# Kernel optimization log

Hardware: AMD Instinct MI355X
Metric: run time of the kernel (lower is better)

## Reference

```python
import jax, jax.numpy as jnp
import numpy as np

N_HEADS = 1
D_MODEL = 128
TOP_K = 64
BATCH = 4
SEQ = 4096


def _rope_tables(T, d_head):
    # div_term = 10000**(arange(0,d,2)/d), repeat_interleave(2); even slice recovers the base freqs
    pos = jnp.arange(T, dtype=jnp.float32)[:, None]            # (T,1)
    div = 10000.0 ** (jnp.arange(0, d_head, 2, dtype=jnp.float32) / d_head)  # (d/2,)
    ang = pos / div[None, :]                                    # (T, d/2)
    return jnp.cos(ang), jnp.sin(ang)


def _apply_rope(x, cos, sin):
    # x: (..., T, d); cos/sin: (T, d/2) broadcast over leading dims
    xe = x[..., 0::2]
    xo = x[..., 1::2]
    re = xe * cos - xo * sin
    ro = xe * sin + xo * cos
    return jnp.stack([re, ro], axis=-1).reshape(x.shape)


def setup_inputs() -> dict:
    key = jax.random.key(0)
    kq, kk, kv = jax.random.split(key, 3)
    q = jax.random.normal(kq, (BATCH, SEQ, D_MODEL), dtype=jnp.float32)
    k = jax.random.normal(kk, (BATCH, SEQ, D_MODEL), dtype=jnp.float32)
    v = jax.random.normal(kv, (BATCH, SEQ, D_MODEL), dtype=jnp.float32)
    return {"q": q, "k": k, "v": v}


def reference(q, k, v):
    b, T, d_model = q.shape
    H = N_HEADS
    D = d_model // H  # d_head; module only valid for H=1 (k is never head-split)
    qh = q.reshape(b, T, H, D).transpose(0, 2, 1, 3)   # (b,H,T,D)
    vh = v.reshape(b, T, H, D).transpose(0, 2, 1, 3)   # (b,H,T,D)
    kh = k[:, None, :, :]                              # (b,1,T,d_model) == (b,H,T,D) for H=1

    cos, sin = _rope_tables(T, D)
    qh = _apply_rope(qh, cos, sin)
    kh = _apply_rope(kh, cos, sin)

    scale = 1.0 / jnp.sqrt(jnp.asarray(D, dtype=qh.dtype))
    logits = jnp.einsum('bhtd,bhsd->bhts', qh, kh) * scale   # (b,H,T,T)

    idx = jnp.arange(T)
    causal = idx[None, :] <= idx[:, None]                    # (T,T): key j <= query i
    logits = jnp.where(causal[None, None], logits, -jnp.inf)

    topk_vals, topk_idx = jax.lax.top_k(logits, TOP_K)       # (b,H,T,K)
    attn = jax.nn.softmax(topk_vals, axis=-1)                # -inf rows -> 0 weight

    bi = jnp.arange(b)[:, None, None, None]
    hi = jnp.arange(H)[None, :, None, None]
    topk_v = vh[bi, hi, topk_idx]                            # (b,H,T,K,D)
    out = jnp.einsum('bhtk,bhtkd->bhtd', attn, topk_v)       # (b,H,T,D)
    return out.transpose(0, 2, 1, 3).reshape(b, T, d_model)
```

## Files before the change

### kernel.cpp

```cpp
#include <hip/hip_runtime.h>
#include <math.h>

#define BATCH 4
#define SEQ   4096
#define DM    128
#define TOPK  64
#define SCALE 0.08838834764831845f
#define CAP   384

typedef short bf16x8 __attribute__((ext_vector_type(8)));
typedef float f32x4  __attribute__((ext_vector_type(4)));

__device__ __forceinline__ unsigned short f2bf(float x) {
    unsigned u = __float_as_uint(x);
    u += 0x7FFFu + ((u >> 16) & 1u);
    return (unsigned short)(u >> 16);
}
__device__ __forceinline__ float bf2f(unsigned short h) {
    return __uint_as_float(((unsigned)h) << 16);
}
__device__ __forceinline__ void split3(float x, unsigned short& h,
                                       unsigned short& md, unsigned short& l) {
    h = f2bf(x);
    float r1 = x - bf2f(h);
    md = f2bf(r1);
    float r2 = r1 - bf2f(md);
    l = f2bf(r2);
}

__device__ __forceinline__ unsigned fmap(float f) {
    unsigned u = __float_as_uint(f);
    return (u & 0x80000000u) ? ~u : (u | 0x80000000u);
}
__device__ __forceinline__ float finv(unsigned u) {
    return (u & 0x80000000u) ? __uint_as_float(u & 0x7FFFFFFFu) : __uint_as_float(~u);
}
__device__ __forceinline__ float wave_fmax(float v) {
    #pragma unroll
    for (int m = 32; m; m >>= 1) v = fmaxf(v, __shfl_xor(v, m));
    return v;
}
__device__ __forceinline__ float wave_fsum(float v) {
    #pragma unroll
    for (int m = 32; m; m >>= 1) v += __shfl_xor(v, m);
    return v;
}
__device__ __forceinline__ int wave_isum(int v) {
    #pragma unroll
    for (int m = 32; m; m >>= 1) v += __shfl_xor(v, m);
    return v;
}
__device__ __forceinline__ unsigned wave_umax(unsigned v) {
    #pragma unroll
    for (int m = 32; m; m >>= 1) { unsigned o = __shfl_xor(v, m); v = (o > v) ? o : v; }
    return v;
}

__global__ void rope_decomp(const float* __restrict__ q, const float* __restrict__ k,
                            unsigned short* __restrict__ qh, unsigned short* __restrict__ qm,
                            unsigned short* __restrict__ ql, unsigned short* __restrict__ kh,
                            unsigned short* __restrict__ km, unsigned short* __restrict__ kl) {
    int idx = blockIdx.x * blockDim.x + threadIdx.x;
    const int total = BATCH * SEQ * (DM / 2);
    if (idx >= total) return;
    int i   = idx & 63;
    int pos = (idx >> 6) & (SEQ - 1);
    int b   = idx >> 18;
    float dv  = powf(10000.0f, (float)(2 * i) / (float)DM);
    float ang = (float)pos / dv;
    float sn, cs;
    sincosf(ang, &sn, &cs);
    size_t base = ((size_t)b * SEQ + pos) * DM + 2 * i;
    float qe = q[base], qo = q[base + 1];
    float ke = k[base], ko = k[base + 1];
    float q0 = (qe * cs - qo * sn) * SCALE, q1 = (qe * sn + qo * cs) * SCALE;
    float k0 = ke * cs - ko * sn,          k1 = ke * sn + ko * cs;
    unsigned short h, m2, l;
    split3(q0, h, m2, l); qh[base] = h;     qm[base] = m2;     ql[base] = l;
    split3(q1, h, m2, l); qh[base + 1] = h; qm[base + 1] = m2; ql[base + 1] = l;
    split3(k0, h, m2, l); kh[base] = h;     km[base] = m2;     kl[base] = l;
    split3(k1, h, m2, l); kh[base + 1] = h; km[base + 1] = m2; kl[base + 1] = l;
}

__launch_bounds__(256, 2)
__global__ void logits_mfma(const unsigned short* __restrict__ qh, const unsigned short* __restrict__ qm,
                            const unsigned short* __restrict__ ql, const unsigned short* __restrict__ kh,
                            const unsigned short* __restrict__ km, const unsigned short* __restrict__ kl,
                            float* __restrict__ lg, int r0, int m, int stride) {
    const int st = blockIdx.x, qt = blockIdx.y, b = blockIdx.z;
    const int Q0 = r0 + qt * 128, S0 = st * 128;
    if (S0 > Q0 + 127) return;
    const int tid = threadIdx.x, lane = tid & 63, w = tid >> 6;
    const int wm = (w >> 1) * 64, wn = (w & 1) * 64;
    if (S0 + wn > Q0 + wm + 63) return;

    const int rA = Q0 + wm + (lane & 15);
    const int rB = S0 + wn + (lane & 15);
    const int dc = (lane >> 4) * 8;

    f32x4 acc[4][4] = {};
    #pragma unroll
    for (int kk = 0; kk < 4; ++kk) {
        const int doff = kk * 32 + dc;
        bf16x8 Ah[4], Am[4], Al[4], Bh[4], Bm[4], Bl[4];
        #pragma unroll
        for (int i = 0; i < 4; ++i) {
            size_t qoff = ((size_t)b * SEQ + rA + i * 16) * DM + doff;
            Ah[i] = *(const bf16x8*)(qh + qoff);
            Am[i] = *(const bf16x8*)(qm + qoff);
            Al[i] = *(const bf16x8*)(ql + qoff);
            size_t koff = ((size_t)b * SEQ + rB + i * 16) * DM + doff;
            Bh[i] = *(const bf16x8*)(kh + koff);
            Bm[i] = *(const bf16x8*)(km + koff);
            Bl[i] = *(const bf16x8*)(kl + koff);
        }
        #pragma unroll
        for (int i = 0; i < 4; ++i)
            #pragma unroll
            for (int j = 0; j < 4; ++j) {
                f32x4 c = acc[i][j];
                c = __builtin_amdgcn_mfma_f32_16x16x32_bf16(Ah[i], Bh[j], c, 0, 0, 0);
                c = __builtin_amdgcn_mfma_f32_16x16x32_bf16(Ah[i], Bm[j], c, 0, 0, 0);
                c = __builtin_amdgcn_mfma_f32_16x16x32_bf16(Am[i], Bh[j], c, 0, 0, 0);
                c = __builtin_amdgcn_mfma_f32_16x16x32_bf16(Ah[i], Bl[j], c, 0, 0, 0);
                c = __builtin_amdgcn_mfma_f32_16x16x32_bf16(Al[i], Bh[j], c, 0, 0, 0);
                c = __builtin_amdgcn_mfma_f32_16x16x32_bf16(Am[i], Bm[j], c, 0, 0, 0);
                acc[i][j] = c;
            }
    }

    const int colb = lane & 15, rowb = (lane >> 4) * 4;
    #pragma unroll
    for (int i = 0; i < 4; ++i) {
        #pragma unroll
        for (int r = 0; r < 4; ++r) {
            int qrow = Q0 + wm + i * 16 + rowb + r;
            size_t base = ((size_t)(b * m + (qrow - r0))) * stride;
            #pragma unroll
            for (int j = 0; j < 4; ++j) {
                int col = S0 + wn + j * 16 + colb;
                if (col <= qrow) lg[base + col] = acc[i][j][r];
            }
        }
    }
}

__launch_bounds__(256)
__global__ void select_out2(const float* __restrict__ lg, const float* __restrict__ v,
                            float* __restrict__ out, int r0, int m, int stride) {
    __shared__ unsigned long long bufK[4][CAP];
    __shared__ float sW[4][TOPK];
    __shared__ int   sI[4][TOPK];
    __shared__ int   cnt[4];

    const int w = threadIdx.x >> 6, lane = threadIdx.x & 63;
    const int x = blockIdx.x * 4 + w, b = blockIdx.y;
    if (x >= m) return;
    const int t = r0 + x, n = t + 1;
    const float* row = lg + ((size_t)(b * m + x)) * stride;
    const float4* row4 = (const float4*)row;
    const int nv4 = n >> 2, rem = n & 3;

    if (n <= TOPK) {
        float val = (lane < n) ? row[lane] : -3.0e38f;
        float M = wave_fmax(val);
        float wgt = (lane < n) ? expf(val - M) : 0.f;
        float S = wave_fsum(wgt);
        sW[w][lane] = wgt;
        float inv = 1.f / S;
        float a0 = 0.f, a1 = 0.f;
        for (int j = 0; j < n; ++j) {
            float wj = sW[w][j];
            size_t base = ((size_t)b * SEQ + j) * DM;
            a0 += wj * v[base + lane];
            a1 += wj * v[base + 64 + lane];
        }
        size_t ob = ((size_t)b * SEQ + t) * DM;
        out[ob + lane] = a0 * inv;
        out[ob + 64 + lane] = a1 * inv;
        return;
    }

    float T;
    if (n <= 300) {
        T = -3.0e38f;
    } else {
        float p  = 128.f / (float)n;
        float tt = sqrtf(-2.f * logf(p));
        T = tt - (2.30753f + 0.27061f * tt) / (1.f + 0.99229f * tt + 0.04481f * tt * tt);
    }

    unsigned um = 0u;
    float Tlo = -3.3e38f, Thi = 3.3e38f;
    int C = 0;
    for (int it = 0; it < 24; ++it) {
        int c = 0;
        unsigned lm = 0u;
        for (int i = lane; i < nv4; i += 64) {
            float4 r4 = row4[i];
            c += (r4.x >= T) + (r4.y >= T) + (r4.z >= T) + (r4.w >= T);
            if (it == 0) {
                unsigned u0 = fmap(r4.x), u1 = fmap(r4.y), u2 = fmap(r4.z), u3 = fmap(r4.w);
                unsigned a = u0 > u1 ? u0 : u1, bb = u2 > u3 ? u2 : u3;
                a = a > bb ? a : bb;
                lm = a > lm ? a : lm;
            }
        }
        if (lane < rem) {
            float val = row[nv4 * 4 + lane];
            c += (val >= T);
            if (it == 0) { unsigned u = fmap(val); lm = u > lm ? u : lm; }
        }
        C = wave_isum(c);
        if (it == 0) um = wave_umax(lm);
        if (C >= TOPK && C <= CAP) break;
        if (C < TOPK) Thi = T; else Tlo = T;
        if (Tlo > -3.2e38f && Thi < 3.2e38f) T = 0.5f * (Tlo + Thi);
        else if (C < TOPK)                   T = T - 0.45f;
        else                                 T = T + 0.35f;
    }
    const float M = finv(um);

    if (lane == 0) cnt[w] = 0;
    for (int i = lane; i < nv4; i += 64) {
        float4 r4 = row4[i];
        int s = i << 2;
        if (r4.x >= T) { int p = atomicAdd(&cnt[w], 1); if (p < CAP) bufK[w][p] = ((unsigned long long)fmap(r4.x) << 32) | (unsigned)(SEQ - s); }
        if (r4.y >= T) { int p = atomicAdd(&cnt[w], 1); if (p < CAP) bufK[w][p] = ((unsigned long long)fmap(r4.y) << 32) | (unsigned)(SEQ - (s + 1)); }
        if (r4.z >= T) { int p = atomicAdd(&cnt[w], 1); if (p < CAP) bufK[w][p] = ((unsigned long long)fmap(r4.z) << 32) | (unsigned)(SEQ - (s + 2)); }
        if (r4.w >= T) { int p = atomicAdd(&cnt[w], 1); if (p < CAP) bufK[w][p] = ((unsigned long long)fmap(r4.w) << 32) | (unsigned)(SEQ - (s + 3)); }
    }
    if (lane < rem) {
        float val = row[nv4 * 4 + lane];
        if (val >= T) { int p = atomicAdd(&cnt[w], 1); if (p < CAP) bufK[w][p] = ((unsigned long long)fmap(val) << 32) | (unsigned)(SEQ - (nv4 * 4 + lane)); }
    }
    int Cw = cnt[w];
    if (Cw > CAP) Cw = CAP;

    for (int c0 = lane; c0 < Cw; c0 += 64) {
        unsigned long long kc = bufK[w][c0];
        int r = 0;
        for (int j = 0; j < Cw; ++j) r += (bufK[w][j] > kc);
        if (r < TOPK) {
            sW[w][r] = expf(finv((unsigned)(kc >> 32)) - M);
            sI[w][r] = SEQ - (int)(kc & 0xFFFFFFFFu);
        }
    }

    float S = wave_fsum(sW[w][lane]);
    float inv = 1.f / S;

    float a0 = 0.f, a1 = 0.f;
    #pragma unroll 4
    for (int j = 0; j < TOPK; ++j) {
        float wj = sW[w][j];
        int idx = sI[w][j];
        size_t base = ((size_t)b * SEQ + idx) * DM;
        a0 += wj * v[base + lane];
        a1 += wj * v[base + 64 + lane];
    }
    size_t ob = ((size_t)b * SEQ + t) * DM;
    out[ob + lane] = a0 * inv;
    out[ob + 64 + lane] = a1 * inv;
}

__global__ void rope_prep(const float* __restrict__ q, const float* __restrict__ k,
                          float* __restrict__ rq, float* __restrict__ rk) {
    int idx = blockIdx.x * blockDim.x + threadIdx.x;
    const int total = BATCH * SEQ * (DM / 2);
    if (idx >= total) return;
    int i   = idx & 63;
    int pos = (idx >> 6) & (SEQ - 1);
    int b   = idx >> 18;
    float dv  = powf(10000.0f, (float)(2 * i) / (float)DM);
    float ang = (float)pos / dv;
    float sn, cs;
    sincosf(ang, &sn, &cs);
    size_t base = ((size_t)b * SEQ + pos) * DM + 2 * i;
    float qe = q[base], qo = q[base + 1];
    float ke = k[base], ko = k[base + 1];
    rq[base]     = qe * cs - qo * sn;
    rq[base + 1] = qe * sn + qo * cs;
    rk[base]     = ke * cs - ko * sn;
    rk[base + 1] = ke * sn + ko * cs;
}

__launch_bounds__(256)
__global__ void topk_attn(const float* __restrict__ rq, const float* __restrict__ rk,
                          const float* __restrict__ v, float* __restrict__ out) {
    __shared__ unsigned umap[SEQ];
    __shared__ float    qs[DM];
    __shared__ int      selIdx[TOPK];
    __shared__ float    selW[TOPK];
    __shared__ int      cnt;
    __shared__ float    redf[4];
    __shared__ int      redi[4];
    __shared__ float    sMax, sSum;

    const int t   = blockIdx.x & (SEQ - 1);
    const int b   = blockIdx.x >> 12;
    const int tid = threadIdx.x;
    const int lane = tid & 63, wid = tid >> 6;
    const int n = t + 1;

    if (tid < DM) qs[tid] = rq[((size_t)b * SEQ + t) * DM + tid];
    if (tid == 0) cnt = 0;
    __syncthreads();

    float lmax = -INFINITY;
    for (int s = tid; s < n; s += 256) {
        const float4* kr = (const float4*)(rk + ((size_t)b * SEQ + s) * DM);
        const float4* qr = (const float4*)qs;
        float acc = 0.f;
        #pragma unroll
        for (int d = 0; d < DM / 4; ++d) {
            float4 kv = kr[d]; float4 qv = qr[d];
            acc += kv.x * qv.x + kv.y * qv.y + kv.z * qv.z + kv.w * qv.w;
        }
        float lgv = acc * SCALE;
        umap[s] = fmap(lgv);
        lmax = fmaxf(lmax, lgv);
    }
    #pragma unroll
    for (int off = 32; off; off >>= 1) lmax = fmaxf(lmax, __shfl_down(lmax, off));
    if (lane == 0) redf[wid] = lmax;
    __syncthreads();
    if (tid == 0) sMax = fmaxf(fmaxf(redf[0], redf[1]), fmaxf(redf[2], redf[3]));
    __syncthreads();
    const float M = sMax;

    const int K = (n < TOPK) ? n : TOPK;
    unsigned thr = 0u;
    if (n > TOPK) {
        unsigned long long lo = 0ull, hi = (unsigned long long)fmap(M);
        while (lo < hi) {
            unsigned long long mid = (lo + hi + 1ull) >> 1;
            unsigned m32 = (unsigned)mid;
            int c = 0;
            for (int s = tid; s < n; s += 256) c += (umap[s] >= m32) ? 1 : 0;
            #pragma unroll
            for (int off = 32; off; off >>= 1) c += __shfl_down(c, off);
            if (lane == 0) redi[wid] = c;
            __syncthreads();
            int tot = redi[0] + redi[1] + redi[2] + redi[3];
            __syncthreads();
            if (tot >= K) lo = mid; else hi = mid - 1ull;
        }
        thr = (unsigned)lo;
    }

    for (int s = tid; s < n; s += 256) {
        if (umap[s] > thr) {
            int p = atomicAdd(&cnt, 1);
            if (p < TOPK) { selIdx[p] = s; selW[p] = expf(finv(umap[s]) - M); }
        }
    }
    __syncthreads();
    for (int s = tid; s < n; s += 256) {
        if (umap[s] == thr) {
            int p = atomicAdd(&cnt, 1);
            if (p < TOPK) { selIdx[p] = s; selW[p] = expf(finv(umap[s]) - M); }
        }
    }
    __syncthreads();
    const int nsel = (cnt < TOPK) ? cnt : TOPK;

    if (tid < 64) {
        float w = (tid < nsel) ? selW[tid] : 0.f;
        #pragma unroll
        for (int off = 32; off; off >>= 1) w += __shfl_down(w, off);
        if (tid == 0) sSum = w;
    }
    __syncthreads();
    const float inv = 1.0f / sSum;

    if (tid < DM) {
        float a = 0.f;
        for (int j = 0; j < nsel; ++j)
            a += selW[j] * v[((size_t)b * SEQ + selIdx[j]) * DM + tid];
        out[((size_t)b * SEQ + t) * DM + tid] = a * inv;
    }
}

extern "C" void kernel_launch(void* const* d_in, const int* in_sizes, int n_in,
                              void* d_out, int out_size, void* d_ws, size_t ws_size,
                              hipStream_t stream) {
    const float* q = (const float*)d_in[0];
    const float* k = (const float*)d_in[1];
    const float* v = (const float*)d_in[2];
    float* out = (float*)d_out;

    const size_t plane = (size_t)BATCH * SEQ * DM;
    const size_t planesBytes = 6 * plane * sizeof(unsigned short);

    long long Wb = (long long)ws_size - (long long)planesBytes;
    int cr0[64], cm[64], nch = 0;
    bool ok = (Wb > 0);
    int r0 = 0;
    while (ok && r0 < SEQ) {
        int m = SEQ - r0;
        while (m >= 128) {
            long long stride = ((r0 + m + 127) / 128) * 128;
            long long bytes = (long long)BATCH * m * stride * 4;
            if (bytes <= Wb) break;
            m -= 128;
        }
        if (m < 128 || nch >= 64) { ok = false; break; }
        cr0[nch] = r0; cm[nch] = m; ++nch;
        r0 += m;
    }

    const int total = BATCH * SEQ * (DM / 2);

    if (!ok) {
        float* rq = (float*)d_ws;
        float* rk = rq + plane;
        hipLaunchKernelGGL(rope_prep, dim3((total + 255) / 256), dim3(256), 0, stream,
                           q, k, rq, rk);
        hipLaunchKernelGGL(topk_attn, dim3(BATCH * SEQ), dim3(256), 0, stream,
                           rq, rk, v, out);
        return;
    }

    unsigned short* qh = (unsigned short*)d_ws;
    unsigned short* qm = qh + plane;
    unsigned short* ql = qm + plane;
    unsigned short* kh = ql + plane;
    unsigned short* km = kh + plane;
    unsigned short* kl = km + plane;
    float* lgbuf = (float*)((char*)d_ws + planesBytes);

    hipLaunchKernelGGL(rope_decomp, dim3((total + 255) / 256), dim3(256), 0, stream,
                       q, k, qh, qm, ql, kh, km, kl);

    for (int c = 0; c < nch; ++c) {
        const int R0 = cr0[c], M = cm[c];
        const int stride = ((R0 + M + 127) / 128) * 128;
        dim3 g1((R0 + M + 127) / 128, M / 128, BATCH);
        hipLaunchKernelGGL(logits_mfma, g1, dim3(256), 0, stream,
                           qh, qm, ql, kh, km, kl, lgbuf, R0, M, stride);
        dim3 g2((M + 3) / 4, BATCH);
        hipLaunchKernelGGL(select_out2, g2, dim3(256), 0, stream,
                           lgbuf, v, out, R0, M, stride);
    }
}
```

Baseline: 247.0 us.

## Stage logits tiles through LDS, fuse threshold search with collection, cap chunk size

The logits MFMA kernel now stages the Q/K hi/mid/lo bf16 planes into swizzled shared memory using direct global-to-LDS loads, so all waves of a block share them instead of each loading its own fragments. It also raises the occupancy hint to three blocks per SIMD and reorders the MFMAs by precision plane. The top-k select kernel merges threshold counting and candidate collection into one pass and uses a quantile-ratio secant update to reach a valid threshold in fewer passes. The host chunking caps each logits chunk at 96 MB, likely to keep it cache-resident, at the cost of more chunks and launches.

```diff
diff --git a/kernel.cpp b/kernel.cpp
--- a/kernel.cpp
+++ b/kernel.cpp
@@ -54,6 +54,12 @@
     #pragma unroll
     for (int m = 32; m; m >>= 1) { unsigned o = __shfl_xor(v, m); v = (o > v) ? o : v; }
     return v;
+}
+
+__device__ __forceinline__ void gld16(const void* g, void* l) {
+    __builtin_amdgcn_global_load_lds(
+        (const __attribute__((address_space(1))) unsigned int*)g,
+        (__attribute__((address_space(3))) unsigned int*)l, 16, 0, 0);
 }
 
 __global__ void rope_decomp(const float* __restrict__ q, const float* __restrict__ k,
@@ -82,7 +88,7 @@
     split3(k1, h, m2, l); kh[base + 1] = h; km[base + 1] = m2; kl[base + 1] = l;
 }
 
-__launch_bounds__(256, 2)
+__launch_bounds__(256, 3)
 __global__ void logits_mfma(const unsigned short* __restrict__ qh, const unsigned short* __restrict__ qm,
                             const unsigned short* __restrict__ ql, const unsigned short* __restrict__ kh,
                             const unsigned short* __restrict__ km, const unsigned short* __restrict__ kl,
@@ -90,45 +96,92 @@
     const int st = blockIdx.x, qt = blockIdx.y, b = blockIdx.z;
     const int Q0 = r0 + qt * 128, S0 = st * 128;
     if (S0 > Q0 + 127) return;
+
+    __shared__ short Asl[3][128 * 32];
+    __shared__ short Bsl[3][128 * 32];
+
     const int tid = threadIdx.x, lane = tid & 63, w = tid >> 6;
     const int wm = (w >> 1) * 64, wn = (w & 1) * 64;
-    if (S0 + wn > Q0 + wm + 63) return;
-
-    const int rA = Q0 + wm + (lane & 15);
-    const int rB = S0 + wn + (lane & 15);
-    const int dc = (lane >> 4) * 8;
+    const bool active = (S0 + wn <= Q0 + wm + 63);
+
+    const unsigned short* qp[3] = { qh, qm, ql };
+    const unsigned short* kp[3] = { kh, km, kl };
+
+    const int srow = lane >> 2;
+    const int sslot = lane & 3;
+    const int sunit = sslot ^ (srow & 3);
+
+    const int frow_a = wm + (lane & 15);
+    const int frow_b = wn + (lane & 15);
+    const int fu     = lane >> 4;
+    const int fswz   = (fu ^ (lane & 3)) * 8;
 
     f32x4 acc[4][4] = {};
-    #pragma unroll
+
     for (int kk = 0; kk < 4; ++kk) {
-        const int doff = kk * 32 + dc;
-        bf16x8 Ah[4], Am[4], Al[4], Bh[4], Bm[4], Bl[4];
-        #pragma unroll
-        for (int i = 0; i < 4; ++i) {
-            size_t qoff = ((size_t)b * SEQ + rA + i * 16) * DM + doff;
-            Ah[i] = *(const bf16x8*)(qh + qoff);
-            Am[i] = *(const bf16x8*)(qm + qoff);
-            Al[i] = *(const bf16x8*)(ql + qoff);
-            size_t koff = ((size_t)b * SEQ + rB + i * 16) * DM + doff;
-            Bh[i] = *(const bf16x8*)(kh + koff);
-            Bm[i] = *(const bf16x8*)(km + koff);
-            Bl[i] = *(const bf16x8*)(kl + koff);
-        }
-        #pragma unroll
-        for (int i = 0; i < 4; ++i)
-            #pragma unroll
-            for (int j = 0; j < 4; ++j) {
-                f32x4 c = acc[i][j];
-                c = __builtin_amdgcn_mfma_f32_16x16x32_bf16(Ah[i], Bh[j], c, 0, 0, 0);
-                c = __builtin_amdgcn_mfma_f32_16x16x32_bf16(Ah[i], Bm[j], c, 0, 0, 0);
-                c = __builtin_amdgcn_mfma_f32_16x16x32_bf16(Am[i], Bh[j], c, 0, 0, 0);
-                c = __builtin_amdgcn_mfma_f32_16x16x32_bf16(Ah[i], Bl[j], c, 0, 0, 0);
-                c = __builtin_amdgcn_mfma_f32_16x16x32_bf16(Al[i], Bh[j], c, 0, 0, 0);
-                c = __builtin_amdgcn_mfma_f32_16x16x32_bf16(Am[i], Bm[j], c, 0, 0, 0);
-                acc[i][j] = c;
+        const int d0 = kk * 32;
+        for (int c = w; c < 48; c += 4) {
+            bool isA = (c < 24);
+            int c2 = isA ? c : c - 24;
+            int p = c2 >> 3, rowbase = (c2 & 7) << 4;
+            int grow = (isA ? Q0 : S0) + rowbase + srow;
+            const unsigned short* src = (isA ? qp[p] : kp[p]) +
+                ((size_t)b * SEQ + grow) * DM + d0 + sunit * 8;
+            short* dst = (isA ? &Asl[p][rowbase * 32] : &Bsl[p][rowbase * 32]);
+            gld16(src, dst);
+        }
+        __syncthreads();
+
+        if (active) {
+            bf16x8 Ah[4], Bh[4];
+            #pragma unroll
+            for (int i = 0; i < 4; ++i) {
+                Ah[i] = *(const bf16x8*)&Asl[0][(frow_a + i * 16) * 32 + fswz];
+                Bh[i] = *(const bf16x8*)&Bsl[0][(frow_b + i * 16) * 32 + fswz];
             }
-    }
-
+            #pragma unroll
+            for (int i = 0; i < 4; ++i)
+                #pragma unroll
+                for (int j = 0; j < 4; ++j)
+                    acc[i][j] = __builtin_amdgcn_mfma_f32_16x16x32_bf16(Ah[i], Bh[j], acc[i][j], 0, 0, 0);
+
+            bf16x8 Am[4], Bm[4];
+            #pragma unroll
+            for (int i = 0; i < 4; ++i) {
+                Am[i] = *(const bf16x8*)&Asl[1][(frow_a + i * 16) * 32 + fswz];
+                Bm[i] = *(const bf16x8*)&Bsl[1][(frow_b + i * 16) * 32 + fswz];
+            }
+            #pragma unroll
+            for (int i = 0; i < 4; ++i)
+                #pragma unroll
+                for (int j = 0; j < 4; ++j) {
+                    f32x4 c = acc[i][j];
+                    c = __builtin_amdgcn_mfma_f32_16x16x32_bf16(Ah[i], Bm[j], c, 0, 0, 0);
+                    c = __builtin_amdgcn_mfma_f32_16x16x32_bf16(Am[i], Bh[j], c, 0, 0, 0);
+                    c = __builtin_amdgcn_mfma_f32_16x16x32_bf16(Am[i], Bm[j], c, 0, 0, 0);
+                    acc[i][j] = c;
+                }
+
+            bf16x8 Al2[4], Bl2[4];
+            #pragma unroll
+            for (int i = 0; i < 4; ++i) {
+                Al2[i] = *(const bf16x8*)&Asl[2][(frow_a + i * 16) * 32 + fswz];
+                Bl2[i] = *(const bf16x8*)&Bsl[2][(frow_b + i * 16) * 32 + fswz];
+            }
+            #pragma unroll
+            for (int i = 0; i < 4; ++i)
+                #pragma unroll
+                for (int j = 0; j < 4; ++j) {
+                    f32x4 c = acc[i][j];
+                    c = __builtin_amdgcn_mfma_f32_16x16x32_bf16(Ah[i], Bl2[j], c, 0, 0, 0);
+                    c = __builtin_amdgcn_mfma_f32_16x16x32_bf16(Al2[i], Bh[j], c, 0, 0, 0);
+                    acc[i][j] = c;
+                }
+        }
+        __syncthreads();
+    }
+
+    if (!active) return;
     const int colb = lane & 15, rowb = (lane >> 4) * 4;
     #pragma unroll
     for (int i = 0; i < 4; ++i) {
@@ -181,61 +234,57 @@
         return;
     }
 
-    float T;
-    if (n <= 300) {
+    float T, zt = 0.f;
+    if (n <= CAP - 32) {
         T = -3.0e38f;
     } else {
         float p  = 128.f / (float)n;
         float tt = sqrtf(-2.f * logf(p));
-        T = tt - (2.30753f + 0.27061f * tt) / (1.f + 0.99229f * tt + 0.04481f * tt * tt);
-    }
-
-    unsigned um = 0u;
+        zt = tt - (2.30753f + 0.27061f * tt) / (1.f + 0.99229f * tt + 0.04481f * tt * tt);
+        T = zt;
+    }
+
     float Tlo = -3.3e38f, Thi = 3.3e38f;
     int C = 0;
-    for (int it = 0; it < 24; ++it) {
-        int c = 0;
+    unsigned um = 0u;
+    for (int it = 0; it < 12; ++it) {
+        if (lane == 0) cnt[w] = 0;
         unsigned lm = 0u;
         for (int i = lane; i < nv4; i += 64) {
             float4 r4 = row4[i];
-            c += (r4.x >= T) + (r4.y >= T) + (r4.z >= T) + (r4.w >= T);
-            if (it == 0) {
-                unsigned u0 = fmap(r4.x), u1 = fmap(r4.y), u2 = fmap(r4.z), u3 = fmap(r4.w);
-                unsigned a = u0 > u1 ? u0 : u1, bb = u2 > u3 ? u2 : u3;
-                a = a > bb ? a : bb;
-                lm = a > lm ? a : lm;
-            }
+            int s = i << 2;
+            if (r4.x >= T) { unsigned u = fmap(r4.x); lm = u > lm ? u : lm; int p = atomicAdd(&cnt[w], 1); if (p < CAP) bufK[w][p] = ((unsigned long long)u << 32) | (unsigned)(SEQ - s); }
+            if (r4.y >= T) { unsigned u = fmap(r4.y); lm = u > lm ? u : lm; int p = atomicAdd(&cnt[w], 1); if (p < CAP) bufK[w][p] = ((unsigned long long)u << 32) | (unsigned)(SEQ - (s + 1)); }
+            if (r4.z >= T) { unsigned u = fmap(r4.z); lm = u > lm ? u : lm; int p = atomicAdd(&cnt[w], 1); if (p < CAP) bufK[w][p] = ((unsigned long long)u << 32) | (unsigned)(SEQ - (s + 2)); }
+            if (r4.w >= T) { unsigned u = fmap(r4.w); lm = u > lm ? u : lm; int p = atomicAdd(&cnt[w], 1); if (p < CAP) bufK[w][p] = ((unsigned long long)u << 32) | (unsigned)(SEQ - (s + 3)); }
         }
         if (lane < rem) {
             float val = row[nv4 * 4 + lane];
-            c += (val >= T);
-            if (it == 0) { unsigned u = fmap(val); lm = u > lm ? u : lm; }
-        }
-        C = wave_isum(c);
-        if (it == 0) um = wave_umax(lm);
+            if (val >= T) { unsigned u = fmap(val); lm = u > lm ? u : lm; int p = atomicAdd(&cnt[w], 1); if (p < CAP) bufK[w][p] = ((unsigned long long)u << 32) | (unsigned)(SEQ - (nv4 * 4 + lane)); }
+        }
+        um = wave_umax(lm);
+        C = cnt[w];
         if (C >= TOPK && C <= CAP) break;
-        if (C < TOPK) Thi = T; else Tlo = T;
-        if (Tlo > -3.2e38f && Thi < 3.2e38f) T = 0.5f * (Tlo + Thi);
-        else if (C < TOPK)                   T = T - 0.45f;
-        else                                 T = T + 0.35f;
+
+        if (C < TOPK) Thi = fminf(Thi, T); else Tlo = fmaxf(Tlo, T);
+        float Tn; bool okc = false;
+        float phat = (float)(C < 1 ? 1 : C) / (float)n;
+        if (phat < 0.45f && T > 0.05f) {
+            float th = sqrtf(-2.f * logf(phat));
+            float zh = th - (2.30753f + 0.27061f * th) / (1.f + 0.99229f * th + 0.04481f * th * th);
+            if (zh > 0.05f) { Tn = T * (zt / zh); okc = true; }
+        }
+        if (!okc || !(Tn > Tlo && Tn < Thi)) {
+            if (Tlo > -3.2e38f && Thi < 3.2e38f) Tn = 0.5f * (Tlo + Thi);
+            else if (C < TOPK)                   Tn = T - 0.5f;
+            else                                 Tn = T + 0.4f;
+        }
+        T = Tn;
     }
     const float M = finv(um);
-
-    if (lane == 0) cnt[w] = 0;
-    for (int i = lane; i < nv4; i += 64) {
-        float4 r4 = row4[i];
-        int s = i << 2;
-        if (r4.x >= T) { int p = atomicAdd(&cnt[w], 1); if (p < CAP) bufK[w][p] = ((unsigned long long)fmap(r4.x) << 32) | (unsigned)(SEQ - s); }
-        if (r4.y >= T) { int p = atomicAdd(&cnt[w], 1); if (p < CAP) bufK[w][p] = ((unsigned long long)fmap(r4.y) << 32) | (unsigned)(SEQ - (s + 1)); }
-        if (r4.z >= T) { int p = atomicAdd(&cnt[w], 1); if (p < CAP) bufK[w][p] = ((unsigned long long)fmap(r4.z) << 32) | (unsigned)(SEQ - (s + 2)); }
-        if (r4.w >= T) { int p = atomicAdd(&cnt[w], 1); if (p < CAP) bufK[w][p] = ((unsigned long long)fmap(r4.w) << 32) | (unsigned)(SEQ - (s + 3)); }
-    }
-    if (lane < rem) {
-        float val = row[nv4 * 4 + lane];
-        if (val >= T) { int p = atomicAdd(&cnt[w], 1); if (p < CAP) bufK[w][p] = ((unsigned long long)fmap(val) << 32) | (unsigned)(SEQ - (nv4 * 4 + lane)); }
-    }
-    int Cw = cnt[w];
-    if (Cw > CAP) Cw = CAP;
+    int Cw = C; if (Cw > CAP) Cw = CAP;
+
+    sW[w][lane] = 0.f; sI[w][lane] = 0;
 
     for (int c0 = lane; c0 < Cw; c0 += 64) {
         unsigned long long kc = bufK[w][c0];
@@ -394,6 +443,7 @@
     const size_t planesBytes = 6 * plane * sizeof(unsigned short);
 
     long long Wb = (long long)ws_size - (long long)planesBytes;
+    const long long CAPB = 96ll << 20;
     int cr0[64], cm[64], nch = 0;
     bool ok = (Wb > 0);
     int r0 = 0;
@@ -402,7 +452,7 @@
         while (m >= 128) {
             long long stride = ((r0 + m + 127) / 128) * 128;
             long long bytes = (long long)BATCH * m * stride * 4;
-            if (bytes <= Wb) break;
+            if (bytes <= Wb && bytes <= CAPB) break;
             m -= 128;
         }
         if (m < 128 || nch >= 64) { ok = false; break; }
```

New measurement: 289.7 us. 17.3% more time.
